# Kernel optimization log

Measured on AMD Instinct MI355X. Metric: run time of the kernel, lower is better.

## Reference

```python
import jax, jax.numpy as jnp
import numpy as np

NEIGHBOUR_NUM = 8  # args.neighbour_num


def _sqrdis_map(x, y):
    # x: [B,M,3], y: [B,N,3] -> [B,M,N] squared distances
    x2 = jnp.sum(x * x, axis=-1)
    y2 = jnp.sum(y * y, axis=-1)
    inner = jnp.einsum('bmd,bnd->bmn', x, y)
    return x2[:, :, None] + y2[:, None, :] - 2.0 * inner


def _chamfer(x, y):
    d = _sqrdis_map(x, y)
    return d.min(axis=2), d.min(axis=1)


def _neighbor_index(v, k):
    # torch.topk(dist, k+1, largest=False) then drop self
    d = _sqrdis_map(v, v)
    idx = jax.lax.top_k(-d, k + 1)[1]  # ascending distance order
    return idx[:, :, 1:]


def _arap(idx, dp, sp):
    B = dp.shape[0]
    bid = jnp.arange(B)[:, None, None]
    dn = dp[bid, idx] - dp[:, :, None, :]  # [B,N,K,3]
    sn = sp[bid, idx] - sp[:, :, None, :]
    dd = jnp.sqrt(jnp.sum(dn * dn, axis=-1) + 1e-5)
    sd = jnp.sqrt(jnp.sum(sn * sn, axis=-1) + 1e-5)
    diff = dd - sd
    return jnp.sum(diff * diff) / B


def setup_inputs() -> dict:
    key = jax.random.key(0)
    ks = jax.random.split(key, 7)
    T, B, N = 3, 4, 4096
    return {
        'phi': jax.random.normal(ks[0], (T, B, 1024), dtype=jnp.float32),
        'point_weight': jax.random.normal(ks[1], (T, B, N, 1), dtype=jnp.float32),
        'deform_rigid_points': 0.5 * jax.random.normal(ks[2], (T, B, N, 3), dtype=jnp.float32),
        'deformation_points': 0.5 * jax.random.normal(ks[3], (T, B, N, 3), dtype=jnp.float32),
        'rigid_matrix': 0.1 * jax.random.normal(ks[4], (T, B, 4, 4), dtype=jnp.float32),
        'source_points': jax.random.uniform(ks[5], (B, N, 3), dtype=jnp.float32, minval=-1.0, maxval=1.0),
        'target_points': jax.random.uniform(ks[6], (B, N, 3), dtype=jnp.float32, minval=-1.0, maxval=1.0),
    }


def reference(phi, point_weight, deform_rigid_points, deformation_points,
              rigid_matrix, source_points, target_points):
    B = source_points.shape[0]
    T = phi.shape[0]  # iter_time = len(phi_list)
    idx = _neighbor_index(source_points, NEIGHBOUR_NUM)
    trans_mask = jnp.zeros((4, 4), dtype=rigid_matrix.dtype).at[0:3, 3].set(1.0)
    total = jnp.asarray(0.0, dtype=source_points.dtype)
    for t in range(T):  # small fixed iter count, structurally distinct stages
        dp = deformation_points[t]
        # loss_on_cd
        d1, d2 = _chamfer(dp, target_points)
        cd = (jnp.sum(d1) + jnp.sum(d2)) * 0.5 / B
        # loss_on_pd (rigid-deformed vs full deformation)
        diff = deform_rigid_points[t] - dp
        pd = jnp.sum(diff * diff) / B
        # loss_on_sparse
        sp = jnp.mean(jnp.abs(point_weight[t]))
        # loss_on_tran
        tr = trans_mask[None] * rigid_matrix[t]
        tran = jnp.sum(tr * tr) / B
        # loss_on_arap
        ar = _arap(idx, dp, source_points)
        total = total + cd + pd + sp + tran + ar
    return total
```

## Files before the change

### kernel.cpp

```cpp
#include <hip/hip_runtime.h>

#define T_ 3
#define B_ 4
#define N_ 4096
#define K_ 8

#define GROUPS 32
#define GRP_KNN 32
#define GRP_CH  12
#define GRP_SZ  45
#define CWIN 512

typedef short bf16x8 __attribute__((ext_vector_type(8)));
typedef float f32x4  __attribute__((ext_vector_type(4)));
typedef float f32x16 __attribute__((ext_vector_type(16)));

template <int NW>
__device__ inline float block_reduce(float v, float* scratch) {
    #pragma unroll
    for (int off = 32; off > 0; off >>= 1) v += __shfl_down(v, off, 64);
    const int lane = threadIdx.x & 63, wid = threadIdx.x >> 6;
    if (lane == 0) scratch[wid] = v;
    __syncthreads();
    float s = 0.f;
    if (threadIdx.x == 0) {
        #pragma unroll
        for (int w = 0; w < NW; ++w) s += scratch[w];
    }
    return s;
}

#define CE_(A, i, j) { unsigned lo_ = min(A[i], A[j]); A[j] = max(A[i], A[j]); A[i] = lo_; }
__device__ inline void sort8(unsigned s[8]) {
    CE_(s,0,1) CE_(s,2,3) CE_(s,4,5) CE_(s,6,7)
    CE_(s,0,2) CE_(s,1,3) CE_(s,4,6) CE_(s,5,7)
    CE_(s,1,2) CE_(s,5,6)
    CE_(s,0,4) CE_(s,1,5) CE_(s,2,6) CE_(s,3,7)
    CE_(s,2,4) CE_(s,3,5)
    CE_(s,1,2) CE_(s,3,4) CE_(s,5,6)
}
__device__ inline void merge_top8(unsigned a[8], const unsigned s[8]) {
    #pragma unroll
    for (int i = 0; i < 8; ++i) a[i] = min(a[i], s[7 - i]);
    CE_(a,0,4) CE_(a,1,5) CE_(a,2,6) CE_(a,3,7)
    CE_(a,0,2) CE_(a,1,3) CE_(a,4,6) CE_(a,5,7)
    CE_(a,0,1) CE_(a,2,3) CE_(a,4,5) CE_(a,6,7)
}

__device__ inline short hi16(float v) { return (short)(__float_as_uint(v) >> 16); }
__device__ inline float residual(float v) {
    return v - __uint_as_float(__float_as_uint(v) & 0xFFFF0000u);
}
__device__ inline unsigned pk2(short a, short b) {
    return (unsigned)(unsigned short)a | ((unsigned)(unsigned short)b << 16);
}
#define BF16_ONE ((short)0x3F80)

__device__ inline void async_ld(const float* g, float* l) {
    __builtin_amdgcn_global_load_lds(
        (const __attribute__((address_space(1))) void*)g,
        (__attribute__((address_space(3))) void*)l,
        4, 0, 0);
}

__global__ __launch_bounds__(256, 6) void mega_kernel(const float* __restrict__ src,
                                                      const float* __restrict__ dp_all,
                                                      const float* __restrict__ tp,
                                                      const float* __restrict__ drp,
                                                      const float* __restrict__ pw,
                                                      const float* __restrict__ rm,
                                                      float* __restrict__ out) {
    __shared__ uint4 smem4[1024];
    __shared__ float raw[CWIN * 3];
    const f32x4 zero4 = {0.f, 0.f, 0.f, 0.f};

    const int g = blockIdx.x / GRP_SZ;
    const int r = blockIdx.x % GRP_SZ;

    if (r < GRP_KNN) {
        const int knn_id = g * GRP_KNN + r;
        uint4* alds = smem4;
        const int b   = knn_id / (N_ / 16);
        const int qt0 = (knn_id % (N_ / 16)) * 16;
        const float* sb = src + (size_t)b * N_ * 3;

        const int wid  = __builtin_amdgcn_readfirstlane(threadIdx.x >> 6);
        const int lane = threadIdx.x & 63;
        const int n    = lane & 15;
        const int quad = lane >> 4;
        const int rbase = quad * 4;
        const int qid  = qt0 + n;

        bf16x8 bfrag = (bf16x8)(short)0;
        {
            float x = sb[3 * qid], y = sb[3 * qid + 1], z = sb[3 * qid + 2];
            float q2 = fmaf(x, x, fmaf(y, y, z * z));
            short hx = hi16(x), hy = hi16(y), hz = hi16(z);
            short lx = hi16(residual(x)), ly = hi16(residual(y)), lz = hi16(residual(z));
            if (quad == 0) bfrag = (bf16x8){hx, hy, hz, hx, hy, hz, BF16_ONE, BF16_ONE};
            else if (quad == 1) bfrag = (bf16x8){lx, ly, lz, lx, ly, lz,
                                                 hi16(q2), hi16(residual(q2))};
        }

        unsigned a[K_];
        #pragma unroll
        for (int p = 0; p < K_; ++p) a[p] = 0xFFFFFFFFu;

        #pragma unroll
        for (int c = 0; c < 6; ++c) {
            const int chunk = c * 4 + wid;
            async_ld(sb + chunk * 64 + lane, raw + chunk * 64);
        }

        for (int w = 0; w < N_ / CWIN; ++w) {
            __syncthreads();
            #pragma unroll
            for (int rr = 0; rr < 2; ++rr) {
                int jloc = rr * 256 + threadIdx.x;
                float x = raw[3 * jloc], y = raw[3 * jloc + 1], z = raw[3 * jloc + 2];
                float p2 = fmaf(x, x, fmaf(y, y, z * z));
                float mx = -2.f * x, my = -2.f * y, mz = -2.f * z;
                short mhx = hi16(mx), mhy = hi16(my), mhz = hi16(mz);
                short mlx = hi16(residual(mx)), mly = hi16(residual(my)), mlz = hi16(residual(mz));
                uint4 f0 = make_uint4(pk2(mhx, mhy), pk2(mhz, mlx), pk2(mly, mlz),
                                      pk2(hi16(p2), hi16(residual(p2))));
                uint4 f1 = make_uint4(f0.x, f0.y, f0.z, pk2(BF16_ONE, BF16_ONE));
                int tile = jloc >> 4, m = jloc & 15;
                alds[tile * 32 + m]      = f0;
                alds[tile * 32 + 16 + m] = f1;
            }
            __syncthreads();

            if (w + 1 < N_ / CWIN) {
                const float* nb = sb + (w + 1) * (CWIN * 3);
                #pragma unroll
                for (int c = 0; c < 6; ++c) {
                    const int chunk = c * 4 + wid;
                    async_ld(nb + chunk * 64 + lane, raw + chunk * 64);
                }
            }

            #pragma unroll
            for (int bt = 0; bt < 4; ++bt) {
                unsigned s8[8];
                #pragma unroll
                for (int h = 0; h < 2; ++h) {
                    const int tile = wid * 8 + bt * 2 + h;
                    const int tbg  = w * CWIN + tile * 16;
                    bf16x8 af = (bf16x8)(short)0;
                    if (quad < 2) {
                        union { uint4 u; bf16x8 v; } cv;
                        cv.u = alds[tile * 32 + quad * 16 + n];
                        af = cv.v;
                    }
                    f32x4 d = __builtin_amdgcn_mfma_f32_16x16x32_bf16(af, bfrag, zero4, 0, 0, 0);
                    #pragma unroll
                    for (int rr = 0; rr < 4; ++rr)
                        s8[h * 4 + rr] = (__float_as_uint(d[rr]) & 0xFFFFF000u)
                                         | (unsigned)(tbg | (rbase + rr));
                    if (tbg == qt0) {
                        #pragma unroll
                        for (int rr = 0; rr < 4; ++rr)
                            if (rbase + rr == n) s8[h * 4 + rr] = 0xFFFFFFFFu;
                    }
                }
                sort8(s8);
                merge_top8(a, s8);
            }
        }

        #pragma unroll
        for (int mk = 16; mk <= 32; mk <<= 1) {
            unsigned t[8];
            #pragma unroll
            for (int e = 0; e < K_; ++e) t[e] = __shfl_xor(a[e], mk, 64);
            merge_top8(a, t);
        }

        __syncthreads();
        unsigned* sm = (unsigned*)smem4;
        unsigned* nidx = (unsigned*)smem4 + 1024;
        if (lane < 16) {
            #pragma unroll
            for (int e = 0; e < K_; ++e) sm[(wid * 16 + n) * 9 + e] = a[e];
        }
        __syncthreads();
        if (threadIdx.x < 16) {
            const int q = threadIdx.x;
            unsigned md[K_];
            #pragma unroll
            for (int e = 0; e < K_; ++e) md[e] = sm[q * 9 + e];
            #pragma unroll
            for (int wv = 1; wv < 4; ++wv) {
                unsigned t[8];
                #pragma unroll
                for (int e = 0; e < K_; ++e) t[e] = sm[(wv * 16 + q) * 9 + e];
                merge_top8(md, t);
            }
            #pragma unroll
            for (int e = 0; e < K_; ++e) nidx[q * 8 + e] = md[e] & 0xFFFu;
        }
        __syncthreads();

        float acc = 0.f;
        if (threadIdx.x < 16 * K_) {
            const int q  = threadIdx.x >> 3;
            const int qi = qt0 + q;
            const int j  = (int)nidx[threadIdx.x];
            float sx = sb[3 * qi], sy = sb[3 * qi + 1], sz = sb[3 * qi + 2];
            float ex = sb[3 * j] - sx, ey = sb[3 * j + 1] - sy, ez = sb[3 * j + 2] - sz;
            float sd = sqrtf(fmaf(ex, ex, fmaf(ey, ey, ez * ez)) + 1e-5f);
            #pragma unroll
            for (int t = 0; t < T_; ++t) {
                const float* dpb = dp_all + ((size_t)(t * B_ + b)) * N_ * 3;
                float dx = dpb[3 * j] - dpb[3 * qi];
                float dy = dpb[3 * j + 1] - dpb[3 * qi + 1];
                float dz = dpb[3 * j + 2] - dpb[3 * qi + 2];
                float dd = sqrtf(fmaf(dx, dx, fmaf(dy, dy, dz * dz)) + 1e-5f);
                float df = dd - sd;
                acc = fmaf(df, df, acc);
            }
        }
        float s = block_reduce<4>(acc, (float*)smem4);
        if (threadIdx.x == 0) atomicAdd(out, s * (1.0f / B_));

    } else if (r < GRP_KNN + GRP_CH) {
        const f32x16 zero16 = {0.f,0.f,0.f,0.f, 0.f,0.f,0.f,0.f,
                               0.f,0.f,0.f,0.f, 0.f,0.f,0.f,0.f};
        uint4* alds = smem4;
        const int cb = g * GRP_CH + (r - GRP_KNN);
        const int tbd  = cb >> 4;
        const int slab = cb & 15;
        const int dir = tbd & 1;
        const int tb  = tbd >> 1;
        const int b = tb % B_, t = tb / B_;

        const float* dpb = dp_all + ((size_t)(t * B_ + b)) * N_ * 3;
        const float* tpb = tp + (size_t)b * N_ * 3;
        const float* cbase = dir ? dpb : tpb;
        const float* qbase = dir ? tpb : dpb;

        const int lane = threadIdx.x & 63;
        const int wid  = __builtin_amdgcn_readfirstlane(threadIdx.x >> 6);
        const int col  = lane & 31;
        const int kg   = lane >> 5;

        bf16x8 bfrag[2];
        #pragma unroll
        for (int s = 0; s < 2; ++s) {
            const int qid = slab * 256 + s * 128 + wid * 32 + col;
            float x = qbase[3 * qid], y = qbase[3 * qid + 1], z = qbase[3 * qid + 2];
            float q2 = fmaf(x, x, fmaf(y, y, z * z));
            short hx = hi16(x), hy = hi16(y), hz = hi16(z);
            short lx = hi16(residual(x)), ly = hi16(residual(y)), lz = hi16(residual(z));
            if (kg == 0) bfrag[s] = (bf16x8){hx, hy, hz, hx, hy, hz, lx, ly};
            else bfrag[s] = (bf16x8){lz, lx, ly, lz, BF16_ONE, BF16_ONE,
                                     hi16(q2), hi16(residual(q2))};
        }

        float run0 = 3.4e38f, run1 = 3.4e38f;

        #pragma unroll
        for (int c = 0; c < 6; ++c) {
            const int chunk = c * 4 + wid;
            async_ld(cbase + chunk * 64 + lane, raw + chunk * 64);
        }

        for (int w = 0; w < N_ / CWIN; ++w) {
            __syncthreads();
            #pragma unroll
            for (int rr = 0; rr < 2; ++rr) {
                int j = rr * 256 + (int)threadIdx.x;
                float x = raw[3 * j], y = raw[3 * j + 1], z = raw[3 * j + 2];
                float p2 = fmaf(x, x, fmaf(y, y, z * z));
                float mx = -2.f * x, my = -2.f * y, mz = -2.f * z;
                short mhx = hi16(mx), mhy = hi16(my), mhz = hi16(mz);
                short mlx = hi16(residual(mx)), mly = hi16(residual(my)), mlz = hi16(residual(mz));
                unsigned w0 = pk2(mhx, mhy), w1 = pk2(mhz, mlx), w2 = pk2(mly, mlz);
                unsigned pw2 = pk2(hi16(p2), hi16(residual(p2)));
                alds[j]       = make_uint4(w0, w1, w2, w0);
                alds[512 + j] = make_uint4(w1, w2, pw2, pk2(BF16_ONE, BF16_ONE));
            }
            __syncthreads();

            if (w + 1 < N_ / CWIN) {
                const float* nb = cbase + (w + 1) * (CWIN * 3);
                #pragma unroll
                for (int c = 0; c < 6; ++c) {
                    const int chunk = c * 4 + wid;
                    async_ld(nb + chunk * 64 + lane, raw + chunk * 64);
                }
            }

            #pragma unroll
            for (int tile = 0; tile < CWIN / 32; ++tile) {
                union { uint4 u; bf16x8 v; } cv;
                cv.u = alds[kg * 512 + tile * 32 + col];
                {
                    f32x16 d = __builtin_amdgcn_mfma_f32_32x32x16_bf16(cv.v, bfrag[0], zero16, 0, 0, 0);
                    float m0 = fminf(fminf(d[0],  d[1]),  fminf(d[2],  d[3]));
                    float m1 = fminf(fminf(d[4],  d[5]),  fminf(d[6],  d[7]));
                    float m2 = fminf(fminf(d[8],  d[9]),  fminf(d[10], d[11]));
                    float m3 = fminf(fminf(d[12], d[13]), fminf(d[14], d[15]));
                    run0 = fminf(run0, fminf(fminf(m0, m1), fminf(m2, m3)));
                }
                {
                    f32x16 d = __builtin_amdgcn_mfma_f32_32x32x16_bf16(cv.v, bfrag[1], zero16, 0, 0, 0);
                    float m0 = fminf(fminf(d[0],  d[1]),  fminf(d[2],  d[3]));
                    float m1 = fminf(fminf(d[4],  d[5]),  fminf(d[6],  d[7]));
                    float m2 = fminf(fminf(d[8],  d[9]),  fminf(d[10], d[11]));
                    float m3 = fminf(fminf(d[12], d[13]), fminf(d[14], d[15]));
                    run1 = fminf(run1, fminf(fminf(m0, m1), fminf(m2, m3)));
                }
            }
        }

        run0 = fminf(run0, __shfl_xor(run0, 32, 64));
        run1 = fminf(run1, __shfl_xor(run1, 32, 64));
        float vsum = (lane < 32) ? (run0 + run1) : 0.f;
        __syncthreads();
        float ssum = block_reduce<4>(vsum, (float*)smem4);
        if (threadIdx.x == 0) atomicAdd(out, ssum * (0.5f / B_));

    } else {
        const int PD_N = T_ * B_ * N_ * 3;
        const int SP_N = T_ * B_ * N_;
        const int stride = GROUPS * 256;
        const int gid = g * 256 + threadIdx.x;
        float apd = 0.f;
        for (int i = gid; i < PD_N; i += stride) {
            float d = drp[i] - dp_all[i];
            apd = fmaf(d, d, apd);
        }
        float asp = 0.f;
        for (int i = gid; i < SP_N; i += stride) asp += fabsf(pw[i]);
        float atr = 0.f;
        if (gid < T_ * B_ * 3) {
            int t = gid / (B_ * 3);
            int b = (gid / 3) % B_;
            int rr = gid % 3;
            float v = rm[t * B_ * 16 + b * 16 + rr * 4 + 3];
            atr = v * v;
        }
        float acc = apd * (1.0f / B_) + asp * (1.0f / (B_ * N_)) + atr * (1.0f / B_);
        float s = block_reduce<4>(acc, (float*)smem4);
        if (threadIdx.x == 0) atomicAdd(out, s);
    }
}

extern "C" void kernel_launch(void* const* d_in, const int* in_sizes, int n_in,
                              void* d_out, int out_size, void* d_ws, size_t ws_size,
                              hipStream_t stream) {
    const float* pw  = (const float*)d_in[1];
    const float* drp = (const float*)d_in[2];
    const float* dp  = (const float*)d_in[3];
    const float* rm  = (const float*)d_in[4];
    const float* sp  = (const float*)d_in[5];
    const float* tp  = (const float*)d_in[6];
    float* out = (float*)d_out;

    hipMemsetAsync(out, 0, sizeof(float), stream);
    mega_kernel<<<GROUPS * GRP_SZ, 256, 0, stream>>>(sp, dp, tp, drp, pw, rm, out);
}
```

Measured before the change: 118.4 us.

## Rebalance block roles: smaller chamfer slabs and fold misc losses into chamfer blocks

Reorganises the grid from 32 groups of 45 blocks into 256 groups of 7 (4 kNN, 3 chamfer). Each chamfer block now handles 128 queries with one MFMA fragment instead of 256 with two, which doubles the chamfer block count. The separate pd/sparse/translation reduction blocks are removed, and that work is spread one element per thread across the chamfer blocks. Occupancy launch bounds rise to 7. The goal is better load balance and fewer tail blocks, at the cost of reloading candidate windows twice as often.

```diff
diff --git a/kernel.cpp b/kernel.cpp
--- a/kernel.cpp
+++ b/kernel.cpp
@@ -5,10 +5,9 @@
 #define N_ 4096
 #define K_ 8
 
-#define GROUPS 32
-#define GRP_KNN 32
-#define GRP_CH  12
-#define GRP_SZ  45
+#define GRP_SZ  7
+#define GRP_KNN 4
+#define GROUPS  256
 #define CWIN 512
 
 typedef short bf16x8 __attribute__((ext_vector_type(8)));
@@ -63,7 +62,7 @@
         4, 0, 0);
 }
 
-__global__ __launch_bounds__(256, 6) void mega_kernel(const float* __restrict__ src,
+__global__ __launch_bounds__(256, 7) void mega_kernel(const float* __restrict__ src,
                                                       const float* __restrict__ dp_all,
                                                       const float* __restrict__ tp,
                                                       const float* __restrict__ drp,
@@ -224,15 +223,15 @@
         float s = block_reduce<4>(acc, (float*)smem4);
         if (threadIdx.x == 0) atomicAdd(out, s * (1.0f / B_));
 
-    } else if (r < GRP_KNN + GRP_CH) {
+    } else {
         const f32x16 zero16 = {0.f,0.f,0.f,0.f, 0.f,0.f,0.f,0.f,
                                0.f,0.f,0.f,0.f, 0.f,0.f,0.f,0.f};
         uint4* alds = smem4;
-        const int cb = g * GRP_CH + (r - GRP_KNN);
-        const int tbd  = cb >> 4;
-        const int slab = cb & 15;
-        const int dir = tbd & 1;
-        const int tb  = tbd >> 1;
+        const int cid   = g * 3 + (r - GRP_KNN);
+        const int combo = cid >> 5;
+        const int slab  = cid & 31;
+        const int dir = combo & 1;
+        const int tb  = combo >> 1;
         const int b = tb % B_, t = tb / B_;
 
         const float* dpb = dp_all + ((size_t)(t * B_ + b)) * N_ * 3;
@@ -245,20 +244,19 @@
         const int col  = lane & 31;
         const int kg   = lane >> 5;
 
-        bf16x8 bfrag[2];
-        #pragma unroll
-        for (int s = 0; s < 2; ++s) {
-            const int qid = slab * 256 + s * 128 + wid * 32 + col;
+        bf16x8 bfrag;
+        {
+            const int qid = slab * 128 + wid * 32 + col;
             float x = qbase[3 * qid], y = qbase[3 * qid + 1], z = qbase[3 * qid + 2];
             float q2 = fmaf(x, x, fmaf(y, y, z * z));
             short hx = hi16(x), hy = hi16(y), hz = hi16(z);
             short lx = hi16(residual(x)), ly = hi16(residual(y)), lz = hi16(residual(z));
-            if (kg == 0) bfrag[s] = (bf16x8){hx, hy, hz, hx, hy, hz, lx, ly};
-            else bfrag[s] = (bf16x8){lz, lx, ly, lz, BF16_ONE, BF16_ONE,
-                                     hi16(q2), hi16(residual(q2))};
-        }
-
-        float run0 = 3.4e38f, run1 = 3.4e38f;
+            if (kg == 0) bfrag = (bf16x8){hx, hy, hz, hx, hy, hz, lx, ly};
+            else bfrag = (bf16x8){lz, lx, ly, lz, BF16_ONE, BF16_ONE,
+                                  hi16(q2), hi16(residual(q2))};
+        }
+
+        float run = 3.4e38f;
 
         #pragma unroll
         for (int c = 0; c < 6; ++c) {
@@ -296,55 +294,38 @@
             for (int tile = 0; tile < CWIN / 32; ++tile) {
                 union { uint4 u; bf16x8 v; } cv;
                 cv.u = alds[kg * 512 + tile * 32 + col];
-                {
-                    f32x16 d = __builtin_amdgcn_mfma_f32_32x32x16_bf16(cv.v, bfrag[0], zero16, 0, 0, 0);
-                    float m0 = fminf(fminf(d[0],  d[1]),  fminf(d[2],  d[3]));
-                    float m1 = fminf(fminf(d[4],  d[5]),  fminf(d[6],  d[7]));
-                    float m2 = fminf(fminf(d[8],  d[9]),  fminf(d[10], d[11]));
-                    float m3 = fminf(fminf(d[12], d[13]), fminf(d[14], d[15]));
-                    run0 = fminf(run0, fminf(fminf(m0, m1), fminf(m2, m3)));
-                }
-                {
-                    f32x16 d = __builtin_amdgcn_mfma_f32_32x32x16_bf16(cv.v, bfrag[1], zero16, 0, 0, 0);
-                    float m0 = fminf(fminf(d[0],  d[1]),  fminf(d[2],  d[3]));
-                    float m1 = fminf(fminf(d[4],  d[5]),  fminf(d[6],  d[7]));
-                    float m2 = fminf(fminf(d[8],  d[9]),  fminf(d[10], d[11]));
-                    float m3 = fminf(fminf(d[12], d[13]), fminf(d[14], d[15]));
-                    run1 = fminf(run1, fminf(fminf(m0, m1), fminf(m2, m3)));
-                }
-            }
-        }
-
-        run0 = fminf(run0, __shfl_xor(run0, 32, 64));
-        run1 = fminf(run1, __shfl_xor(run1, 32, 64));
-        float vsum = (lane < 32) ? (run0 + run1) : 0.f;
+                f32x16 d = __builtin_amdgcn_mfma_f32_32x32x16_bf16(cv.v, bfrag, zero16, 0, 0, 0);
+                float m0 = fminf(fminf(d[0],  d[1]),  fminf(d[2],  d[3]));
+                float m1 = fminf(fminf(d[4],  d[5]),  fminf(d[6],  d[7]));
+                float m2 = fminf(fminf(d[8],  d[9]),  fminf(d[10], d[11]));
+                float m3 = fminf(fminf(d[12], d[13]), fminf(d[14], d[15]));
+                run = fminf(run, fminf(fminf(m0, m1), fminf(m2, m3)));
+            }
+        }
+
+        run = fminf(run, __shfl_xor(run, 32, 64));
+        float contrib = (lane < 32) ? run * (0.5f / B_) : 0.f;
+
+        {
+            const int PD_N = T_ * B_ * N_ * 3;
+            const int SP_N = T_ * B_ * N_;
+            const int gid = cid * 256 + (int)threadIdx.x;
+            if (gid < PD_N) {
+                float d2 = drp[gid] - dp_all[gid];
+                contrib = fmaf(d2 * (1.0f / B_), d2, contrib);
+            }
+            if (gid < SP_N) contrib += fabsf(pw[gid]) * (1.0f / (B_ * N_));
+            if (gid < T_ * B_ * 3) {
+                int tt = gid / (B_ * 3);
+                int b2 = (gid / 3) % B_;
+                int rr = gid % 3;
+                float v = rm[tt * B_ * 16 + b2 * 16 + rr * 4 + 3];
+                contrib = fmaf(v * (1.0f / B_), v, contrib);
+            }
+        }
         __syncthreads();
-        float ssum = block_reduce<4>(vsum, (float*)smem4);
-        if (threadIdx.x == 0) atomicAdd(out, ssum * (0.5f / B_));
-
-    } else {
-        const int PD_N = T_ * B_ * N_ * 3;
-        const int SP_N = T_ * B_ * N_;
-        const int stride = GROUPS * 256;
-        const int gid = g * 256 + threadIdx.x;
-        float apd = 0.f;
-        for (int i = gid; i < PD_N; i += stride) {
-            float d = drp[i] - dp_all[i];
-            apd = fmaf(d, d, apd);
-        }
-        float asp = 0.f;
-        for (int i = gid; i < SP_N; i += stride) asp += fabsf(pw[i]);
-        float atr = 0.f;
-        if (gid < T_ * B_ * 3) {
-            int t = gid / (B_ * 3);
-            int b = (gid / 3) % B_;
-            int rr = gid % 3;
-            float v = rm[t * B_ * 16 + b * 16 + rr * 4 + 3];
-            atr = v * v;
-        }
-        float acc = apd * (1.0f / B_) + asp * (1.0f / (B_ * N_)) + atr * (1.0f / B_);
-        float s = block_reduce<4>(acc, (float*)smem4);
-        if (threadIdx.x == 0) atomicAdd(out, s);
+        float ssum = block_reduce<4>(contrib, (float*)smem4);
+        if (threadIdx.x == 0) atomicAdd(out, ssum);
     }
 }
 
```

Result: faster. 116.0 us (-2.0%).
